# Kernel tuning notes

Hardware: AMD Instinct MI355X
Metric: run time of the kernel (lower is better)

## Reference

```python
import jax, jax.numpy as jnp
from jax import lax
import numpy as np

BN_EPS = 1e-3  # Keras BatchNormalization default epsilon

@jax.custom_vjp
def ste_sign(x):
    # larq ste_sign: sign with sign(0)=+1
    return jnp.where(x >= 0, 1.0, -1.0).astype(x.dtype)

def _ste_fwd(x):
    return ste_sign(x), x

def _ste_bwd(x, g):
    # straight-through estimator: pass grad where |x| <= 1
    return (g * (jnp.abs(x) <= 1.0).astype(g.dtype),)

ste_sign.defvjp(_ste_fwd, _ste_bwd)

def setup_inputs() -> dict:
    key = jax.random.key(0)
    ks = jax.random.split(key, 6)
    x = jax.random.normal(ks[0], (64, 2048, 128), dtype=jnp.float32)
    kernel = jax.random.normal(ks[1], (3, 128, 256), dtype=jnp.float32) * 0.05
    bias = jax.random.normal(ks[2], (256,), dtype=jnp.float32) * 0.01
    beta = jax.random.normal(ks[3], (256,), dtype=jnp.float32) * 0.01
    moving_mean = jax.random.normal(ks[4], (256,), dtype=jnp.float32) * 0.1
    moving_var = jax.random.uniform(ks[5], (256,), dtype=jnp.float32) + 0.5  # positive
    return {"x": x, "kernel": kernel, "bias": bias, "beta": beta,
            "moving_mean": moving_mean, "moving_var": moving_var}

def reference(x, kernel, bias, beta, moving_mean, moving_var):
    # QuantConv1D: binarize input and kernel, then valid conv, stride 1
    xq = ste_sign(x)                 # [B, T, Cin]
    kq = ste_sign(kernel)            # [K, Cin, Cout]
    y = lax.conv_general_dilated(
        xq, kq, window_strides=(1,), padding='VALID',
        dimension_numbers=('NWC', 'WIO', 'NWC'))  # [B, T-K+1, Cout]
    y = y + bias
    # BatchNormalization, inference mode (training=False), scale=False -> no gamma
    inv = lax.rsqrt(moving_var + BN_EPS)
    return (y - moving_mean) * inv + beta
```

## Files before the change

### kernel.cpp

```cpp
#include <hip/hip_runtime.h>
#include <hip/hip_bf16.h>
#include <stdint.h>


#define B 64
#define T 2048
#define CIN 128
#define COUT 256
#define KW 3
#define TOUT (T - KW + 1)
#define TCHUNK 66
#define CHUNKS 31
#define NROWS (TCHUNK + KW - 1)

__global__ __launch_bounds__(256) void pack_w_kernel(const float* __restrict__ ker,
                                                     const float* __restrict__ bias,
                                                     const float* __restrict__ beta,
                                                     const float* __restrict__ mean,
                                                     const float* __restrict__ var,
                                                     uint32_t* __restrict__ kb32,
                                                     float* __restrict__ A,
                                                     float* __restrict__ C) {
    int k  = blockIdx.x >> 2;
    int q  = blockIdx.x & 3;
    int co = threadIdx.x;
    uint32_t w = 0;
    const float* src = ker + ((size_t)k * CIN + q * 32) * COUT + co;
    #pragma unroll 8
    for (int i = 0; i < 32; ++i) {
        if (src[(size_t)i * COUT] >= 0.0f) w |= (1u << i);
    }
    kb32[(size_t)(k * 4 + q) * COUT + co] = w;
    if (k == 0 && q == 0) {
        float inv = 1.0f / sqrtf(var[co] + 1e-3f);
        A[co] = -2.0f * inv;
        C[co] = (384.0f + bias[co] - mean[co]) * inv + beta[co];
    }
}

__global__ __launch_bounds__(256) void conv_fused_kernel(const float* __restrict__ x,
                                                         const uint32_t* __restrict__ kb32,
                                                         const float* __restrict__ A,
                                                         const float* __restrict__ C,
                                                         float* __restrict__ out) {
    const int co    = threadIdx.x;
    const int chunk = blockIdx.x;
    const int b     = chunk / CHUNKS;
    const int t0    = (chunk % CHUNKS) * TCHUNK;

    __shared__ __align__(16) ulonglong2 xs[NROWS];

    {
        const int wid  = threadIdx.x >> 6;
        const int lane = threadIdx.x & 63;
        const float* xrow = x + ((size_t)b * T + t0) * CIN;
        #pragma unroll 4
        for (int i = 0; i < NROWS / 4; ++i) {
            int r = wid * (NROWS / 4) + i;
            float v0 = xrow[(size_t)r * CIN + lane];
            float v1 = xrow[(size_t)r * CIN + 64 + lane];
            uint64_t m0 = __ballot(v0 >= 0.0f);
            uint64_t m1 = __ballot(v1 >= 0.0f);
            if (lane == 0) { xs[r].x = m0; xs[r].y = m1; }
        }
    }

    const uint32_t* kc = kb32 + co;
    uint64_t k00 = (uint64_t)kc[0 * COUT] | ((uint64_t)kc[1 * COUT] << 32);
    uint64_t k01 = (uint64_t)kc[2 * COUT] | ((uint64_t)kc[3 * COUT] << 32);
    uint64_t k10 = (uint64_t)kc[4 * COUT] | ((uint64_t)kc[5 * COUT] << 32);
    uint64_t k11 = (uint64_t)kc[6 * COUT] | ((uint64_t)kc[7 * COUT] << 32);
    uint64_t k20 = (uint64_t)kc[8 * COUT] | ((uint64_t)kc[9 * COUT] << 32);
    uint64_t k21 = (uint64_t)kc[10 * COUT] | ((uint64_t)kc[11 * COUT] << 32);
    const float a = A[co];
    const float c = C[co];

    __syncthreads();

    float* orow = out + ((size_t)b * TOUT + t0) * COUT + co;
    ulonglong2 r0 = xs[0];
    ulonglong2 r1 = xs[1];
    #pragma unroll 3
    for (int t = 0; t < TCHUNK; t += 2) {
        ulonglong2 r2 = xs[t + 2];
        ulonglong2 r3 = xs[t + 3];
        int p0 = __popcll(r0.x ^ k00) + __popcll(r0.y ^ k01)
               + __popcll(r1.x ^ k10) + __popcll(r1.y ^ k11)
               + __popcll(r2.x ^ k20) + __popcll(r2.y ^ k21);
        int p1 = __popcll(r1.x ^ k00) + __popcll(r1.y ^ k01)
               + __popcll(r2.x ^ k10) + __popcll(r2.y ^ k11)
               + __popcll(r3.x ^ k20) + __popcll(r3.y ^ k21);
        orow[(size_t)t * COUT]       = fmaf((float)p0, a, c);
        orow[(size_t)(t + 1) * COUT] = fmaf((float)p1, a, c);
        r0 = r2;
        r1 = r3;
    }
}

extern "C" void kernel_launch(void* const* d_in, const int* in_sizes, int n_in,
                              void* d_out, int out_size, void* d_ws, size_t ws_size,
                              hipStream_t stream) {
    const float* x    = (const float*)d_in[0];
    const float* ker  = (const float*)d_in[1];
    const float* bias = (const float*)d_in[2];
    const float* beta = (const float*)d_in[3];
    const float* mean = (const float*)d_in[4];
    const float* var  = (const float*)d_in[5];
    float* out = (float*)d_out;

    uint32_t* kb32 = (uint32_t*)d_ws;
    float*    A    = (float*)(kb32 + (size_t)KW * 4 * COUT);
    float*    C    = A + COUT;

    pack_w_kernel<<<KW * 4, 256, 0, stream>>>(ker, bias, beta, mean, var, kb32, A, C);
    conv_fused_kernel<<<B * CHUNKS, 256, 0, stream>>>(x, kb32, A, C, out);
}
```

Before: 50.60 us.

## Vectorize x loads and output stores with float4 and permuted bit packing

Input rows are now loaded as float4, with a strided channel-to-bit permutation so that four ballots per wave produce two packed rows. Each thread now computes four output channels per time step and writes them as float4. The time range is split across the four waves instead of every thread walking all 66 steps. The goals are fewer global load and store instructions and wider memory transactions, at the cost of more registers for the 12 uint4 kernel words per thread.

```diff
diff --git a/kernel.cpp b/kernel.cpp
--- a/kernel.cpp
+++ b/kernel.cpp
@@ -1,5 +1,4 @@
 #include <hip/hip_runtime.h>
-#include <hip/hip_bf16.h>
 #include <stdint.h>
 
 
@@ -13,6 +12,11 @@
 #define CHUNKS 31
 #define NROWS (TCHUNK + KW - 1)
 
+__device__ __forceinline__ int popc_row(uint4 r, uint4 k) {
+    return __popc(r.x ^ k.x) + __popc(r.y ^ k.y) +
+           __popc(r.z ^ k.z) + __popc(r.w ^ k.w);
+}
+
 __global__ __launch_bounds__(256) void pack_w_kernel(const float* __restrict__ ker,
                                                      const float* __restrict__ bias,
                                                      const float* __restrict__ beta,
@@ -22,16 +26,16 @@
                                                      float* __restrict__ A,
                                                      float* __restrict__ C) {
     int k  = blockIdx.x >> 2;
-    int q  = blockIdx.x & 3;
+    int i  = blockIdx.x & 3;
     int co = threadIdx.x;
-    uint32_t w = 0;
-    const float* src = ker + ((size_t)k * CIN + q * 32) * COUT + co;
+    const float* src = ker + ((size_t)(k * CIN + i)) * COUT + co;
+    uint32_t wbits = 0;
     #pragma unroll 8
-    for (int i = 0; i < 32; ++i) {
-        if (src[(size_t)i * COUT] >= 0.0f) w |= (1u << i);
+    for (int bb = 0; bb < 32; ++bb) {
+        if (src[(size_t)(4 * bb) * COUT] >= 0.0f) wbits |= (1u << bb);
     }
-    kb32[(size_t)(k * 4 + q) * COUT + co] = w;
-    if (k == 0 && q == 0) {
+    kb32[(size_t)(k * 4 + i) * COUT + co] = wbits;
+    if (blockIdx.x == 0) {
         float inv = 1.0f / sqrtf(var[co] + 1e-3f);
         A[co] = -2.0f * inv;
         C[co] = (384.0f + bias[co] - mean[co]) * inv + beta[co];
@@ -43,55 +47,83 @@
                                                          const float* __restrict__ A,
                                                          const float* __restrict__ C,
                                                          float* __restrict__ out) {
-    const int co    = threadIdx.x;
+    const int tid = threadIdx.x;
+    const int wv  = tid >> 6;
+    const int l   = tid & 63;
     const int chunk = blockIdx.x;
     const int b     = chunk / CHUNKS;
     const int t0    = (chunk % CHUNKS) * TCHUNK;
 
-    __shared__ __align__(16) ulonglong2 xs[NROWS];
+    __shared__ uint4 xs[NROWS];
 
-    {
-        const int wid  = threadIdx.x >> 6;
-        const int lane = threadIdx.x & 63;
-        const float* xrow = x + ((size_t)b * T + t0) * CIN;
-        #pragma unroll 4
-        for (int i = 0; i < NROWS / 4; ++i) {
-            int r = wid * (NROWS / 4) + i;
-            float v0 = xrow[(size_t)r * CIN + lane];
-            float v1 = xrow[(size_t)r * CIN + 64 + lane];
-            uint64_t m0 = __ballot(v0 >= 0.0f);
-            uint64_t m1 = __ballot(v1 >= 0.0f);
-            if (lane == 0) { xs[r].x = m0; xs[r].y = m1; }
+    const float* xbase = x + ((size_t)b * T + t0) * CIN;
+    for (int rd = wv; rd < NROWS / 2; rd += 4) {
+        float4 v = *(const float4*)(xbase + (size_t)rd * 256 + l * 4);
+        uint64_t m0 = __ballot(v.x >= 0.0f);
+        uint64_t m1 = __ballot(v.y >= 0.0f);
+        uint64_t m2 = __ballot(v.z >= 0.0f);
+        uint64_t m3 = __ballot(v.w >= 0.0f);
+        if (l == 0) {
+            xs[rd * 2] = make_uint4((uint32_t)m0, (uint32_t)m1,
+                                    (uint32_t)m2, (uint32_t)m3);
+        } else if (l == 1) {
+            xs[rd * 2 + 1] = make_uint4((uint32_t)(m0 >> 32), (uint32_t)(m1 >> 32),
+                                        (uint32_t)(m2 >> 32), (uint32_t)(m3 >> 32));
         }
     }
 
-    const uint32_t* kc = kb32 + co;
-    uint64_t k00 = (uint64_t)kc[0 * COUT] | ((uint64_t)kc[1 * COUT] << 32);
-    uint64_t k01 = (uint64_t)kc[2 * COUT] | ((uint64_t)kc[3 * COUT] << 32);
-    uint64_t k10 = (uint64_t)kc[4 * COUT] | ((uint64_t)kc[5 * COUT] << 32);
-    uint64_t k11 = (uint64_t)kc[6 * COUT] | ((uint64_t)kc[7 * COUT] << 32);
-    uint64_t k20 = (uint64_t)kc[8 * COUT] | ((uint64_t)kc[9 * COUT] << 32);
-    uint64_t k21 = (uint64_t)kc[10 * COUT] | ((uint64_t)kc[11 * COUT] << 32);
-    const float a = A[co];
-    const float c = C[co];
+    const int co0 = l * 4;
+    uint4 kw_raw[KW][4];
+    #pragma unroll
+    for (int k = 0; k < KW; ++k)
+        #pragma unroll
+        for (int i = 0; i < 4; ++i)
+            kw_raw[k][i] = *(const uint4*)(kb32 + (size_t)(k * 4 + i) * COUT + co0);
+    uint4 kj[4][KW];
+    #pragma unroll
+    for (int j = 0; j < 4; ++j)
+        #pragma unroll
+        for (int k = 0; k < KW; ++k)
+            kj[j][k] = make_uint4(((const uint32_t*)&kw_raw[k][0])[j],
+                                  ((const uint32_t*)&kw_raw[k][1])[j],
+                                  ((const uint32_t*)&kw_raw[k][2])[j],
+                                  ((const uint32_t*)&kw_raw[k][3])[j]);
+    const float4 av = *(const float4*)(A + co0);
+    const float4 cv = *(const float4*)(C + co0);
 
     __syncthreads();
 
-    float* orow = out + ((size_t)b * TOUT + t0) * COUT + co;
-    ulonglong2 r0 = xs[0];
-    ulonglong2 r1 = xs[1];
-    #pragma unroll 3
-    for (int t = 0; t < TCHUNK; t += 2) {
-        ulonglong2 r2 = xs[t + 2];
-        ulonglong2 r3 = xs[t + 3];
-        int p0 = __popcll(r0.x ^ k00) + __popcll(r0.y ^ k01)
-               + __popcll(r1.x ^ k10) + __popcll(r1.y ^ k11)
-               + __popcll(r2.x ^ k20) + __popcll(r2.y ^ k21);
-        int p1 = __popcll(r1.x ^ k00) + __popcll(r1.y ^ k01)
-               + __popcll(r2.x ^ k10) + __popcll(r2.y ^ k11)
-               + __popcll(r3.x ^ k20) + __popcll(r3.y ^ k21);
-        orow[(size_t)t * COUT]       = fmaf((float)p0, a, c);
-        orow[(size_t)(t + 1) * COUT] = fmaf((float)p1, a, c);
+    const int tstart = (wv == 0) ? 0 : 18 + (wv - 1) * 16;
+    const int tlen   = (wv == 0) ? 18 : 16;
+
+    float* orow = out + ((size_t)b * TOUT + t0 + tstart) * COUT + co0;
+    uint4 r0 = xs[tstart];
+    uint4 r1 = xs[tstart + 1];
+    #pragma unroll 2
+    for (int tt = 0; tt < tlen; tt += 2) {
+        uint4 r2 = xs[tstart + tt + 2];
+        uint4 r3 = xs[tstart + tt + 3];
+        float4 o0, o1;
+        int p;
+        p = popc_row(r0, kj[0][0]) + popc_row(r1, kj[0][1]) + popc_row(r2, kj[0][2]);
+        o0.x = fmaf((float)p, av.x, cv.x);
+        p = popc_row(r1, kj[0][0]) + popc_row(r2, kj[0][1]) + popc_row(r3, kj[0][2]);
+        o1.x = fmaf((float)p, av.x, cv.x);
+        p = popc_row(r0, kj[1][0]) + popc_row(r1, kj[1][1]) + popc_row(r2, kj[1][2]);
+        o0.y = fmaf((float)p, av.y, cv.y);
+        p = popc_row(r1, kj[1][0]) + popc_row(r2, kj[1][1]) + popc_row(r3, kj[1][2]);
+        o1.y = fmaf((float)p, av.y, cv.y);
+        p = popc_row(r0, kj[2][0]) + popc_row(r1, kj[2][1]) + popc_row(r2, kj[2][2]);
+        o0.z = fmaf((float)p, av.z, cv.z);
+        p = popc_row(r1, kj[2][0]) + popc_row(r2, kj[2][1]) + popc_row(r3, kj[2][2]);
+        o1.z = fmaf((float)p, av.z, cv.z);
+        p = popc_row(r0, kj[3][0]) + popc_row(r1, kj[3][1]) + popc_row(r2, kj[3][2]);
+        o0.w = fmaf((float)p, av.w, cv.w);
+        p = popc_row(r1, kj[3][0]) + popc_row(r2, kj[3][1]) + popc_row(r3, kj[3][2]);
+        o1.w = fmaf((float)p, av.w, cv.w);
+
+        *(float4*)(orow + (size_t)tt * COUT)       = o0;
+        *(float4*)(orow + (size_t)(tt + 1) * COUT) = o1;
         r0 = r2;
         r1 = r3;
     }
```

Measured after the change: 56.08 us. 10.8% more time.
